# Optimization experiments

Measured on AMD Instinct MI355X. Metric: run time of the kernel, lower is better.

Reference implementation:

```python
import jax, jax.numpy as jnp
from jax import lax
import numpy as np

# ---- SLAYER SRM-alpha neuron / simulation constants (net_params) ----
THETA = 10.0      # spiking threshold
TAU_SR = 1.0      # PSP (synaptic response) time constant
TAU_REF = 1.0     # refractory time constant
TS = 1.0          # simulation timestep
POOL_GAIN = 1.1 * THETA  # SLAYER pool layer uses fixed weights = 1.1*theta (sum pool)

# SRM alpha kernel eps[n] = (n*Ts/tau) * exp(1 - n*Ts/tau) = c * n * d^n with
#   d = exp(-Ts/tau), c = e*Ts/tau.  Causal convolution with this kernel obeys
# a 2nd-order linear recurrence, so we implement psp as a lax.scan over time
# (the "recursive exponential temporal filter" the original does via temporal conv).

def psp(x):
    """Alpha-kernel temporal filter along last (time) axis."""
    d = float(np.exp(-TS / TAU_SR))
    c = float(np.e * TS / TAU_SR)
    xt = jnp.moveaxis(x, -1, 0)  # (T, ...)
    z = jnp.zeros_like(xt[0])
    def step(carry, u):
        p, q = carry
        q = d * (q + p)       # q[t] = sum_{n>=1} n d^n x[t-n]
        p = d * p + u         # p[t] = sum_{n>=0} d^n x[t-n]
        return (p, q), c * q
    _, y = lax.scan(step, (z, z), xt)
    return jnp.moveaxis(y, 0, -1)


def spike(u):
    """SLAYER spike generation: threshold the membrane potential at theta and
    subtract a refractory alpha kernel (-2*theta * alpha(tauRef)) from the
    future potential after each spike. Sequential scan over time."""
    d = float(np.exp(-TS / TAU_REF))
    c_r = float(-2.0 * THETA * np.e * TS / TAU_REF)
    ut = jnp.moveaxis(u, -1, 0)  # (T, ...)
    z = jnp.zeros_like(ut[0])
    def step(carry, u_t):
        p, q = carry
        q = d * (q + p)                       # refractory filter state
        s = (u_t + c_r * q >= THETA).astype(u_t.dtype)
        p = d * p + s                         # spikes feed the refractory filter
        return (p, q), s
    _, s = lax.scan(step, (z, z), ut)
    return jnp.moveaxis(s, 0, -1) / TS


def pool(x, k):
    """SLAYER pool: conv with fixed weight 1.1*theta (sum pool scaled)."""
    B, C, H, W, T = x.shape
    xr = x.reshape(B, C, H // k, k, W // k, k, T)
    return POOL_GAIN * xr.sum(axis=(3, 5))


def conv2d_t(x, W, pad):
    """Per-timestep 2D conv (SLAYER conv has time-kernel 1, no bias)."""
    B, C, H, Wd, T = x.shape
    xf = jnp.moveaxis(x, -1, 1).reshape(B * T, C, H, Wd)
    y = lax.conv_general_dilated(xf, W, (1, 1), [(pad, pad), (pad, pad)],
                                 dimension_numbers=('NCHW', 'OIHW', 'NCHW'))
    O, Ho, Wo = y.shape[1], y.shape[2], y.shape[3]
    return jnp.moveaxis(y.reshape(B, T, O, Ho, Wo), 1, -1)


def setup_inputs() -> dict:
    key = jax.random.key(0)
    ks = jax.random.split(key, 5)
    B, T = 8, 300
    s_in = jax.random.bernoulli(ks[0], 0.1, (B, 2, 128, 128, T)).astype(jnp.float32)
    # weightScale 10/50/... only affects init magnitude; choose scales that
    # produce non-degenerate spiking activity.
    W1 = jax.random.normal(ks[1], (16, 2, 5, 5), jnp.float32) * 0.5
    W2 = jax.random.normal(ks[2], (32, 16, 3, 3), jnp.float32) * 0.2
    Wf1 = jax.random.normal(ks[3], (512, 32, 8, 8), jnp.float32) * 0.05
    Wf2 = jax.random.normal(ks[4], (11, 512), jnp.float32) * 0.2
    return {"s_in": s_in, "W1": W1, "W2": W2, "Wf1": Wf1, "Wf2": Wf2}


def reference(s_in, W1, W2, Wf1, Wf2):
    s = spike(psp(pool(s_in, 4)))                 # SP0: (B,2,32,32,T)
    s = spike(psp(conv2d_t(s, W1, 2)))            # SC1: (B,16,32,32,T)
    s = spike(psp(pool(s, 2)))                    # SP1: (B,16,16,16,T)
    # SDC dropout p=0.0 -> identity
    s = spike(psp(conv2d_t(s, W2, 1)))            # SC2: (B,32,16,16,T)
    s = spike(psp(pool(s, 2)))                    # SP2: (B,32,8,8,T)
    # SDF dropout p=0.0 -> identity
    s = spike(psp(jnp.einsum('bchwt,ochw->bot', s, Wf1)))  # SF1: (B,512,T)
    s = spike(psp(jnp.einsum('bct,oc->bot', s, Wf2)))      # SF2: (B,11,T)
    return s
```

## Files before the change

### kernel.cpp

```cpp
#include <hip/hip_runtime.h>
#include <stdint.h>

#define T_STEPS 300
#define T4 75

typedef __attribute__((ext_vector_type(8))) short bf16x8;
typedef __attribute__((ext_vector_type(4))) float f32x4;

__device__ __forceinline__ void scan_step(float x, float& pp, float& pq,
                                          float& rp, float& rq, float& s_out) {
    const float D  = 0.36787944117144233f;
    const float C  = 2.7182818284590452f;
    const float CR = -54.365636569180904f;
    const float TH = 10.0f;
    pq = D * (pq + pp);
    pp = D * pp + x;
    float u = C * pq;
    rq = D * (rq + rp);
    float s = (u + CR * rq >= TH) ? 1.0f : 0.0f;
    rp = D * rp + s;
    s_out = s;
}

#define SCAN4(v, PACK)                                                     \
    {                                                                      \
        float s0, s1, s2, s3;                                              \
        scan_step(v.x, pp, pq, rp, rq, s0);                                \
        scan_step(v.y, pp, pq, rp, rq, s1);                                \
        scan_step(v.z, pp, pq, rp, rq, s2);                                \
        scan_step(v.w, pp, pq, rp, rq, s3);                                \
        PACK = (uint32_t)s0 | ((uint32_t)s1 << 8) |                        \
               ((uint32_t)s2 << 16) | ((uint32_t)s3 << 24);                \
    }

#define FMA4(A, wc) A.x = fmaf(wc, f0, A.x); A.y = fmaf(wc, f1, A.y); \
                    A.z = fmaf(wc, f2, A.z); A.w = fmaf(wc, f3, A.w);

__global__ __launch_bounds__(256) void k_pool4(const float* __restrict__ in,
                                               float* __restrict__ z) {
    int idx = blockIdx.x * 256 + threadIdx.x;
    int t4 = idx % T4;
    int n  = idx / T4;
    int x = n & 31, y = (n >> 5) & 31, bc = n >> 10;
    const float* base = in + ((size_t)bc * 16384 + (size_t)(4 * y) * 128 + 4 * x) * T_STEPS + 4 * t4;
    float4 acc = {0.f, 0.f, 0.f, 0.f};
#pragma unroll
    for (int i = 0; i < 4; ++i)
#pragma unroll
        for (int j = 0; j < 4; ++j) {
            float4 v = *reinterpret_cast<const float4*>(base + ((size_t)i * 128 + j) * T_STEPS);
            acc.x += v.x; acc.y += v.y; acc.z += v.z; acc.w += v.w;
        }
    float4 o = {11.f * acc.x, 11.f * acc.y, 11.f * acc.z, 11.f * acc.w};
    *reinterpret_cast<float4*>(z + (size_t)n * T_STEPS + 4 * t4) = o;
}

__global__ __launch_bounds__(256) void k_scan_l0(const float* __restrict__ z,
                                                 uint32_t* __restrict__ sp, int N) {
    int n = blockIdx.x * 256 + threadIdx.x;
    if (n >= N) return;
    const float4* zp = reinterpret_cast<const float4*>(z + (size_t)n * T_STEPS);
    float pp = 0.f, pq = 0.f, rp = 0.f, rq = 0.f;
#pragma unroll 2
    for (int t4 = 0; t4 < T4; ++t4) {
        float4 v = zp[t4];
        uint32_t pack;
        SCAN4(v, pack);
        sp[(size_t)t4 * N + n] = pack;
    }
}

__global__ __launch_bounds__(256) void k_scan_plane(const float4* __restrict__ z,
                                                    uint32_t* __restrict__ sp, int N) {
    int n = blockIdx.x * 256 + threadIdx.x;
    if (n >= N) return;
    float pp = 0.f, pq = 0.f, rp = 0.f, rq = 0.f;
#pragma unroll 2
    for (int t4 = 0; t4 < T4; ++t4) {
        float4 v = z[(size_t)t4 * N + n];
        uint32_t pack;
        SCAN4(v, pack);
        sp[(size_t)t4 * N + n] = pack;
    }
}

__global__ __launch_bounds__(256) void k_scan_f32(const float* __restrict__ z,
                                                  float* __restrict__ s, int N, int ostride) {
    int n = blockIdx.x * blockDim.x + threadIdx.x;
    if (n >= N) return;
    const float4* zp = reinterpret_cast<const float4*>(z + (size_t)n * T_STEPS);
    float* spo = s + (size_t)n * ostride;
    float pp = 0.f, pq = 0.f, rp = 0.f, rq = 0.f;
    for (int it = 0; it < T4; ++it) {
        float4 v = zp[it];
        float4 o;
        scan_step(v.x, pp, pq, rp, rq, o.x);
        scan_step(v.y, pp, pq, rp, rq, o.y);
        scan_step(v.z, pp, pq, rp, rq, o.z);
        scan_step(v.w, pp, pq, rp, rq, o.w);
        *reinterpret_cast<float4*>(spo + it * 4) = o;
    }
}

template<int HW, int NIN, int NOUT>
__global__ __launch_bounds__(256) void k_pool2s(const uint32_t* __restrict__ sin,
                                                uint32_t* __restrict__ sout) {
    int n = blockIdx.x * 256 + threadIdx.x;
    if (n >= NOUT) return;
    int x = n % HW, y = (n / HW) % HW, bc = n / (HW * HW);
    const int W2d = HW * 2;
    const uint32_t* base0 = sin + (size_t)bc * W2d * W2d + (size_t)(2 * y) * W2d + 2 * x;
    float pp = 0.f, pq = 0.f, rp = 0.f, rq = 0.f;
#pragma unroll 2
    for (int t4 = 0; t4 < T4; ++t4) {
        const uint32_t* p = base0 + (size_t)t4 * NIN;
        uint32_t sum = p[0] + p[1] + p[W2d] + p[W2d + 1];
        float4 v;
        v.x = 11.f * (float)(sum & 0xffu);
        v.y = 11.f * (float)((sum >> 8) & 0xffu);
        v.z = 11.f * (float)((sum >> 16) & 0xffu);
        v.w = 11.f * (float)(sum >> 24);
        uint32_t pack;
        SCAN4(v, pack);
        sout[(size_t)t4 * NOUT + n] = pack;
    }
}

__global__ __launch_bounds__(256) void k_pool2s_bf(const uint32_t* __restrict__ sin,
                                                   ushort* __restrict__ sb) {
    int n = blockIdx.x * 256 + threadIdx.x;
    if (n >= 16384) return;
    int x = n & 7, y = (n >> 3) & 7, bc = n >> 6;
    const uint32_t* base0 = sin + (size_t)bc * 256 + (size_t)(2 * y) * 16 + 2 * x;
    int b = n >> 11, k = n & 2047;
    ushort* out = sb + (size_t)b * 320 * 2048 + k;
    float pp = 0.f, pq = 0.f, rp = 0.f, rq = 0.f;
    for (int t4 = 0; t4 < T4; ++t4) {
        const uint32_t* p = base0 + (size_t)t4 * 65536;
        uint32_t sum = p[0] + p[1] + p[16] + p[17];
        float4 v;
        v.x = 11.f * (float)(sum & 0xffu);
        v.y = 11.f * (float)((sum >> 8) & 0xffu);
        v.z = 11.f * (float)((sum >> 16) & 0xffu);
        v.w = 11.f * (float)(sum >> 24);
        float s0, s1, s2, s3;
        scan_step(v.x, pp, pq, rp, rq, s0);
        scan_step(v.y, pp, pq, rp, rq, s1);
        scan_step(v.z, pp, pq, rp, rq, s2);
        scan_step(v.w, pp, pq, rp, rq, s3);
        out[(size_t)(t4 * 4 + 0) * 2048] = s0 != 0.f ? 0x3F80 : 0;
        out[(size_t)(t4 * 4 + 1) * 2048] = s1 != 0.f ? 0x3F80 : 0;
        out[(size_t)(t4 * 4 + 2) * 2048] = s2 != 0.f ? 0x3F80 : 0;
        out[(size_t)(t4 * 4 + 3) * 2048] = s3 != 0.f ? 0x3F80 : 0;
    }
}

__global__ __launch_bounds__(256) void k_conv1(const uint32_t* __restrict__ s0p,
                                               const float* __restrict__ W1,
                                               float4* __restrict__ z1p) {
    __shared__ float w_lds[2][25][16];
    int bid = blockIdx.x;
    int pixblk = bid & 3;
    int t4 = (bid >> 2) % 75;
    int b  = bid / 300;
    int tid = threadIdx.x;
    for (int j = tid; j < 800; j += 256) {
        int o = j & 15, kk = (j >> 4) % 25, c = j / 400;
        w_lds[c][kk][o] = W1[(o * 2 + c) * 25 + kk];
    }
    __syncthreads();
    int pix = pixblk * 256 + tid;
    int px = pix & 31, py = pix >> 5;
    float4 acc[16];
#pragma unroll
    for (int o = 0; o < 16; ++o) acc[o] = make_float4(0.f, 0.f, 0.f, 0.f);
    const uint32_t* pb = s0p + (size_t)t4 * 16384 + (size_t)(b * 2) * 1024;
    for (int c = 0; c < 2; ++c) {
#pragma unroll
        for (int ky = 0; ky < 5; ++ky) {
            int yy = py + ky - 2;
            bool rok = (unsigned)yy < 32u;
#pragma unroll
            for (int kx = 0; kx < 5; ++kx) {
                int xx = px + kx - 2;
                uint32_t v = 0;
                if (rok && (unsigned)xx < 32u) v = pb[c * 1024 + yy * 32 + xx];
                float f0 = (float)(v & 0xffu), f1 = (float)((v >> 8) & 0xffu);
                float f2 = (float)((v >> 16) & 0xffu), f3 = (float)(v >> 24);
                int kk = ky * 5 + kx;
#pragma unroll
                for (int oo = 0; oo < 4; ++oo) {
                    float4 w4 = *reinterpret_cast<const float4*>(&w_lds[c][kk][oo * 4]);
                    FMA4(acc[oo * 4 + 0], w4.x);
                    FMA4(acc[oo * 4 + 1], w4.y);
                    FMA4(acc[oo * 4 + 2], w4.z);
                    FMA4(acc[oo * 4 + 3], w4.w);
                }
            }
        }
    }
    size_t zb = (size_t)t4 * 131072 + (size_t)(b * 16) * 1024 + pix;
#pragma unroll
    for (int o = 0; o < 16; ++o) z1p[zb + o * 1024] = acc[o];
}

__global__ __launch_bounds__(256) void k_conv2(const uint32_t* __restrict__ s2p,
                                               const float* __restrict__ W2,
                                               float4* __restrict__ z2p) {
    __shared__ float w_lds[16][9][16];
    int bid = blockIdx.x;
    int oh = bid & 1;
    int t4 = (bid >> 1) % 75;
    int b  = bid / 150;
    int tid = threadIdx.x;
    for (int j = tid; j < 2304; j += 256) {
        int o = j & 15;
        int t9 = (j >> 4) % 9;
        int c  = j / 144;
        w_lds[c][t9][o] = W2[(size_t)((oh * 16 + o) * 16 + c) * 9 + t9];
    }
    __syncthreads();
    int px = tid & 15, py = tid >> 4;
    float4 acc[16];
#pragma unroll
    for (int o = 0; o < 16; ++o) acc[o] = make_float4(0.f, 0.f, 0.f, 0.f);
    const uint32_t* pb = s2p + (size_t)t4 * 32768 + (size_t)(b * 16) * 256;
    for (int c = 0; c < 16; ++c) {
#pragma unroll
        for (int ky = 0; ky < 3; ++ky) {
            int yy = py + ky - 1;
            bool rok = (unsigned)yy < 16u;
#pragma unroll
            for (int kx = 0; kx < 3; ++kx) {
                int xx = px + kx - 1;
                uint32_t v = 0;
                if (rok && (unsigned)xx < 16u) v = pb[c * 256 + yy * 16 + xx];
                float f0 = (float)(v & 0xffu), f1 = (float)((v >> 8) & 0xffu);
                float f2 = (float)((v >> 16) & 0xffu), f3 = (float)(v >> 24);
                int t9 = ky * 3 + kx;
#pragma unroll
                for (int oo = 0; oo < 4; ++oo) {
                    float4 w4 = *reinterpret_cast<const float4*>(&w_lds[c][t9][oo * 4]);
                    FMA4(acc[oo * 4 + 0], w4.x);
                    FMA4(acc[oo * 4 + 1], w4.y);
                    FMA4(acc[oo * 4 + 2], w4.z);
                    FMA4(acc[oo * 4 + 3], w4.w);
                }
            }
        }
    }
    size_t zb = (size_t)t4 * 65536 + (size_t)(b * 32 + oh * 16) * 256 + tid;
#pragma unroll
    for (int o = 0; o < 16; ++o) z2p[zb + o * 256] = acc[o];
}

__device__ __forceinline__ ushort f2bf(float f) {
    uint32_t u = __float_as_uint(f);
    u = u + 0x7fffu + ((u >> 16) & 1u);
    return (ushort)(u >> 16);
}
__device__ __forceinline__ float bf2f(ushort h) {
    return __uint_as_float((uint32_t)h << 16);
}
__global__ __launch_bounds__(256) void k_wsplit(const float* __restrict__ W,
                                                ushort* __restrict__ Wh,
                                                ushort* __restrict__ Wm,
                                                ushort* __restrict__ Wl, int n) {
    int i = blockIdx.x * 256 + threadIdx.x;
    if (i >= n) return;
    float w = W[i];
    ushort h = f2bf(w);
    float r1 = w - bf2f(h);
    ushort m = f2bf(r1);
    float r2 = r1 - bf2f(m);
    ushort l = f2bf(r2);
    Wh[i] = h; Wm[i] = m; Wl[i] = l;
}

__device__ __forceinline__ bf16x8 ldb(const ushort* p) {
    return *reinterpret_cast<const bf16x8*>(p);
}
__global__ __launch_bounds__(256) void k_fc1_mfma(const ushort* __restrict__ Wh,
                                                  const ushort* __restrict__ Wm,
                                                  const ushort* __restrict__ Wl,
                                                  const ushort* __restrict__ sb,
                                                  float* __restrict__ z) {
    int tid = threadIdx.x, lane = tid & 63, wv = tid >> 6;
    int l15 = lane & 15, l4 = lane >> 4;
    int oA = blockIdx.x * 64 + (wv & 1) * 32 + l15;
    int t  = blockIdx.y * 32 + (wv >> 1) * 16 + l15;
    int b  = blockIdx.z;
    size_t a0 = (size_t)oA * 2048 + l4 * 8;
    size_t a1 = a0 + 16 * 2048;
    size_t bo = ((size_t)b * 320 + t) * 2048 + l4 * 8;

    f32x4 acc0 = {0.f, 0.f, 0.f, 0.f};
    f32x4 acc1 = {0.f, 0.f, 0.f, 0.f};

    bf16x8 h0 = ldb(Wh + a0), h1 = ldb(Wh + a1);
    bf16x8 m0 = ldb(Wm + a0), m1 = ldb(Wm + a1);
    bf16x8 l0 = ldb(Wl + a0), l1 = ldb(Wl + a1);
    bf16x8 bb = ldb(sb + bo);

    for (int ks = 0; ks < 64; ++ks) {
        int kn = (ks < 63) ? (ks + 1) * 32 : 0;
        bf16x8 nh0 = ldb(Wh + a0 + kn), nh1 = ldb(Wh + a1 + kn);
        bf16x8 nm0 = ldb(Wm + a0 + kn), nm1 = ldb(Wm + a1 + kn);
        bf16x8 nl0 = ldb(Wl + a0 + kn), nl1 = ldb(Wl + a1 + kn);
        bf16x8 nbb = ldb(sb + bo + kn);
        acc0 = __builtin_amdgcn_mfma_f32_16x16x32_bf16(h0, bb, acc0, 0, 0, 0);
        acc1 = __builtin_amdgcn_mfma_f32_16x16x32_bf16(h1, bb, acc1, 0, 0, 0);
        acc0 = __builtin_amdgcn_mfma_f32_16x16x32_bf16(m0, bb, acc0, 0, 0, 0);
        acc1 = __builtin_amdgcn_mfma_f32_16x16x32_bf16(m1, bb, acc1, 0, 0, 0);
        acc0 = __builtin_amdgcn_mfma_f32_16x16x32_bf16(l0, bb, acc0, 0, 0, 0);
        acc1 = __builtin_amdgcn_mfma_f32_16x16x32_bf16(l1, bb, acc1, 0, 0, 0);
        h0 = nh0; h1 = nh1; m0 = nm0; m1 = nm1; l0 = nl0; l1 = nl1; bb = nbb;
    }

    if (t < T_STEPS) {
        int orow = blockIdx.x * 64 + (wv & 1) * 32 + l4 * 4;
        float* zr = z + ((size_t)b * 512 + orow) * T_STEPS + t;
        zr[0 * T_STEPS] = acc0.x;  zr[1 * T_STEPS] = acc0.y;
        zr[2 * T_STEPS] = acc0.z;  zr[3 * T_STEPS] = acc0.w;
        float* zr2 = zr + 16 * T_STEPS;
        zr2[0 * T_STEPS] = acc1.x; zr2[1 * T_STEPS] = acc1.y;
        zr2[2 * T_STEPS] = acc1.z; zr2[3 * T_STEPS] = acc1.w;
    }
}

__global__ __launch_bounds__(256) void k_fc2(const float* __restrict__ s5,
                                             const float* __restrict__ Wf2,
                                             float* __restrict__ z) {
    int idx = blockIdx.x * 256 + threadIdx.x;
    if (idx >= 6600) return;
    int t4 = idx % T4;
    int r  = idx / T4;
    int b = r & 7, o = r >> 3;
    const float* sp = s5 + (size_t)b * 512 * T_STEPS + 4 * t4;
    const float* wp = Wf2 + (size_t)o * 512;
    float a0 = 0.f, a1 = 0.f, a2 = 0.f, a3 = 0.f;
#pragma unroll 2
    for (int k = 0; k < 512; k += 4) {
        float4 wv = *reinterpret_cast<const float4*>(wp + k);
        float4 v0 = *reinterpret_cast<const float4*>(sp + (size_t)(k + 0) * T_STEPS);
        float4 v1 = *reinterpret_cast<const float4*>(sp + (size_t)(k + 1) * T_STEPS);
        float4 v2 = *reinterpret_cast<const float4*>(sp + (size_t)(k + 2) * T_STEPS);
        float4 v3 = *reinterpret_cast<const float4*>(sp + (size_t)(k + 3) * T_STEPS);
        a0 = fmaf(wv.x, v0.x, a0); a1 = fmaf(wv.x, v0.y, a1); a2 = fmaf(wv.x, v0.z, a2); a3 = fmaf(wv.x, v0.w, a3);
        a0 = fmaf(wv.y, v1.x, a0); a1 = fmaf(wv.y, v1.y, a1); a2 = fmaf(wv.y, v1.z, a2); a3 = fmaf(wv.y, v1.w, a3);
        a0 = fmaf(wv.z, v2.x, a0); a1 = fmaf(wv.z, v2.y, a1); a2 = fmaf(wv.z, v2.z, a2); a3 = fmaf(wv.z, v2.w, a3);
        a0 = fmaf(wv.w, v3.x, a0); a1 = fmaf(wv.w, v3.y, a1); a2 = fmaf(wv.w, v3.z, a2); a3 = fmaf(wv.w, v3.w, a3);
    }
    *reinterpret_cast<float4*>(z + (size_t)(b * 11 + o) * T_STEPS + 4 * t4) = make_float4(a0, a1, a2, a3);
}

__global__ void k_zero(float* out, int n) {
    int i = blockIdx.x * 256 + threadIdx.x;
    if (i < n) out[i] = 0.f;
}

extern "C" void kernel_launch(void* const* d_in, const int* in_sizes, int n_in,
                              void* d_out, int out_size, void* d_ws, size_t ws_size,
                              hipStream_t stream) {
    const float* s_in = (const float*)d_in[0];
    const float* W1   = (const float*)d_in[1];
    const float* W2   = (const float*)d_in[2];
    const float* Wf1  = (const float*)d_in[3];
    const float* Wf2  = (const float*)d_in[4];
    float* out = (float*)d_out;

    const size_t OFF_Z  = 0;
    const size_t OFF_S0 = 157286400;
    const size_t OFF_S1 = 162201600;
    const size_t OFF_S2 = 201523200;
    const size_t OFF_S3 = 211353600;
    const size_t OFF_SB = 231014400;
    const size_t OFF_S5 = 241500160;
    const size_t OFF_WH = 246415360;
    const size_t OFF_WM = 248512512;
    const size_t OFF_WL = 250609664;
    const size_t NEEDED = 252706816;

    if (ws_size < NEEDED) {
        k_zero<<<(26400 + 255) / 256, 256, 0, stream>>>(out, 26400);
        return;
    }

    char* ws = (char*)d_ws;
    float*    Z   = (float*)(ws + OFF_Z);
    uint32_t* s0p = (uint32_t*)(ws + OFF_S0);
    uint32_t* s1p = (uint32_t*)(ws + OFF_S1);
    uint32_t* s2p = (uint32_t*)(ws + OFF_S2);
    uint32_t* s3p = (uint32_t*)(ws + OFF_S3);
    ushort*   sbf = (ushort*)(ws + OFF_SB);
    float*    s5  = (float*)(ws + OFF_S5);
    ushort*   Wh  = (ushort*)(ws + OFF_WH);
    ushort*   Wm  = (ushort*)(ws + OFF_WM);
    ushort*   Wl  = (ushort*)(ws + OFF_WL);

    k_wsplit<<<4096, 256, 0, stream>>>(Wf1, Wh, Wm, Wl, 512 * 2048);

    k_pool4<<<4800, 256, 0, stream>>>(s_in, Z);
    k_scan_l0<<<64, 256, 0, stream>>>(Z, s0p, 16384);

    k_conv1<<<2400, 256, 0, stream>>>(s0p, W1, (float4*)Z);
    k_scan_plane<<<512, 256, 0, stream>>>((const float4*)Z, s1p, 131072);

    k_pool2s<16, 131072, 32768><<<128, 256, 0, stream>>>(s1p, s2p);

    k_conv2<<<1200, 256, 0, stream>>>(s2p, W2, (float4*)Z);
    k_scan_plane<<<256, 256, 0, stream>>>((const float4*)Z, s3p, 65536);

    k_pool2s_bf<<<64, 256, 0, stream>>>(s3p, sbf);

    k_fc1_mfma<<<dim3(8, 10, 8), 256, 0, stream>>>(Wh, Wm, Wl, sbf, Z);
    k_scan_f32<<<16, 256, 0, stream>>>(Z, s5, 4096, 300);

    k_fc2<<<26, 256, 0, stream>>>(s5, Wf2, Z);
    k_scan_f32<<<1, 128, 0, stream>>>(Z, out, 88, 300);
}
```

Baseline: 989.6 us.

## Store FC1 weights and spikes in MFMA fragment order for coalesced loads

The FC1 weight split kernel and the last pool/spike kernel now write their bf16 outputs directly in the per-lane MFMA fragment layout. Each wave then reads a contiguous 1KB chunk per k-step instead of strided rows. The FC1 kernel is retiled so each wave computes 16 outputs by 32 timesteps, sharing the three weight fragments across two spike tiles rather than sharing one spike tile across two weight rows. The aim is better coalescing and less load traffic per MFMA. In exchange, the pool kernel's scattered 2-byte stores become more strided, and the workspace is assumed to have room for 20 padded time tiles.

Measured after the change: 889.0 us. -10.2%, faster.

```diff
diff --git a/kernel.cpp b/kernel.cpp
--- a/kernel.cpp
+++ b/kernel.cpp
@@ -127,13 +127,14 @@
 }
 
 __global__ __launch_bounds__(256) void k_pool2s_bf(const uint32_t* __restrict__ sin,
-                                                   ushort* __restrict__ sb) {
+                                                   ushort* __restrict__ sf) {
     int n = blockIdx.x * 256 + threadIdx.x;
     if (n >= 16384) return;
     int x = n & 7, y = (n >> 3) & 7, bc = n >> 6;
     const uint32_t* base0 = sin + (size_t)bc * 256 + (size_t)(2 * y) * 16 + 2 * x;
     int b = n >> 11, k = n & 2047;
-    ushort* out = sb + (size_t)b * 320 * 2048 + k;
+    size_t kpart = ((size_t)(k >> 5)) * 512 + (size_t)((k >> 3) & 3) * 128 + (k & 7);
+    ushort* outb = sf + (size_t)b * 20 * 64 * 512 + kpart;
     float pp = 0.f, pq = 0.f, rp = 0.f, rq = 0.f;
     for (int t4 = 0; t4 < T4; ++t4) {
         const uint32_t* p = base0 + (size_t)t4 * 65536;
@@ -148,10 +149,13 @@
         scan_step(v.y, pp, pq, rp, rq, s1);
         scan_step(v.z, pp, pq, rp, rq, s2);
         scan_step(v.w, pp, pq, rp, rq, s3);
-        out[(size_t)(t4 * 4 + 0) * 2048] = s0 != 0.f ? 0x3F80 : 0;
-        out[(size_t)(t4 * 4 + 1) * 2048] = s1 != 0.f ? 0x3F80 : 0;
-        out[(size_t)(t4 * 4 + 2) * 2048] = s2 != 0.f ? 0x3F80 : 0;
-        out[(size_t)(t4 * 4 + 3) * 2048] = s3 != 0.f ? 0x3F80 : 0;
+        float sv[4] = {s0, s1, s2, s3};
+#pragma unroll
+        for (int r = 0; r < 4; ++r) {
+            int t = t4 * 4 + r;
+            outb[((size_t)(t >> 4) * 64) * 512 + (size_t)(t & 15) * 8] =
+                sv[r] != 0.f ? (ushort)0x3F80 : (ushort)0;
+        }
     }
 }
 
@@ -262,69 +266,80 @@
 __device__ __forceinline__ float bf2f(ushort h) {
     return __uint_as_float((uint32_t)h << 16);
 }
-__global__ __launch_bounds__(256) void k_wsplit(const float* __restrict__ W,
-                                                ushort* __restrict__ Wh,
-                                                ushort* __restrict__ Wm,
-                                                ushort* __restrict__ Wl, int n) {
+__global__ __launch_bounds__(256) void k_wfrag(const float* __restrict__ W,
+                                               ushort* __restrict__ Wf) {
     int i = blockIdx.x * 256 + threadIdx.x;
-    if (i >= n) return;
+    int o = i >> 11, k = i & 2047;
     float w = W[i];
     ushort h = f2bf(w);
     float r1 = w - bf2f(h);
     ushort m = f2bf(r1);
     float r2 = r1 - bf2f(m);
     ushort l = f2bf(r2);
-    Wh[i] = h; Wm[i] = m; Wl[i] = l;
+    int lane = (((k >> 3) & 3) << 4) | (o & 15);
+    size_t base = (((size_t)(o >> 4)) * 64 + (k >> 5)) * 512 + lane * 8 + (k & 7);
+    const size_t PL = (size_t)32 * 64 * 512;
+    Wf[base] = h;
+    Wf[PL + base] = m;
+    Wf[2 * PL + base] = l;
 }
 
 __device__ __forceinline__ bf16x8 ldb(const ushort* p) {
     return *reinterpret_cast<const bf16x8*>(p);
 }
-__global__ __launch_bounds__(256) void k_fc1_mfma(const ushort* __restrict__ Wh,
-                                                  const ushort* __restrict__ Wm,
-                                                  const ushort* __restrict__ Wl,
-                                                  const ushort* __restrict__ sb,
+__global__ __launch_bounds__(256) void k_fc1_frag(const ushort* __restrict__ Wf,
+                                                  const ushort* __restrict__ sf,
                                                   float* __restrict__ z) {
-    int tid = threadIdx.x, lane = tid & 63, wv = tid >> 6;
+    int wv = threadIdx.x >> 6, lane = threadIdx.x & 63;
+    int gw = blockIdx.x * 4 + wv;
+    int R  = gw & 31;
+    int combo = gw >> 5;
+    int tp = combo % 10, b = combo / 10;
     int l15 = lane & 15, l4 = lane >> 4;
-    int oA = blockIdx.x * 64 + (wv & 1) * 32 + l15;
-    int t  = blockIdx.y * 32 + (wv >> 1) * 16 + l15;
-    int b  = blockIdx.z;
-    size_t a0 = (size_t)oA * 2048 + l4 * 8;
-    size_t a1 = a0 + 16 * 2048;
-    size_t bo = ((size_t)b * 320 + t) * 2048 + l4 * 8;
+
+    const size_t PL = (size_t)32 * 64 * 512;
+    const ushort* A0p = Wf + ((size_t)R * 64) * 512 + lane * 8;
+    const ushort* A1p = A0p + PL;
+    const ushort* A2p = A0p + 2 * PL;
+    const ushort* B0p = sf + ((size_t)(b * 20 + 2 * tp + 0) * 64) * 512 + lane * 8;
+    const ushort* B1p = B0p + (size_t)64 * 512;
 
     f32x4 acc0 = {0.f, 0.f, 0.f, 0.f};
     f32x4 acc1 = {0.f, 0.f, 0.f, 0.f};
 
-    bf16x8 h0 = ldb(Wh + a0), h1 = ldb(Wh + a1);
-    bf16x8 m0 = ldb(Wm + a0), m1 = ldb(Wm + a1);
-    bf16x8 l0 = ldb(Wl + a0), l1 = ldb(Wl + a1);
-    bf16x8 bb = ldb(sb + bo);
+    bf16x8 a0 = ldb(A0p), a1 = ldb(A1p), a2 = ldb(A2p);
+    bf16x8 b0 = ldb(B0p), b1 = ldb(B1p);
 
     for (int ks = 0; ks < 64; ++ks) {
-        int kn = (ks < 63) ? (ks + 1) * 32 : 0;
-        bf16x8 nh0 = ldb(Wh + a0 + kn), nh1 = ldb(Wh + a1 + kn);
-        bf16x8 nm0 = ldb(Wm + a0 + kn), nm1 = ldb(Wm + a1 + kn);
-        bf16x8 nl0 = ldb(Wl + a0 + kn), nl1 = ldb(Wl + a1 + kn);
-        bf16x8 nbb = ldb(sb + bo + kn);
-        acc0 = __builtin_amdgcn_mfma_f32_16x16x32_bf16(h0, bb, acc0, 0, 0, 0);
-        acc1 = __builtin_amdgcn_mfma_f32_16x16x32_bf16(h1, bb, acc1, 0, 0, 0);
-        acc0 = __builtin_amdgcn_mfma_f32_16x16x32_bf16(m0, bb, acc0, 0, 0, 0);
-        acc1 = __builtin_amdgcn_mfma_f32_16x16x32_bf16(m1, bb, acc1, 0, 0, 0);
-        acc0 = __builtin_amdgcn_mfma_f32_16x16x32_bf16(l0, bb, acc0, 0, 0, 0);
-        acc1 = __builtin_amdgcn_mfma_f32_16x16x32_bf16(l1, bb, acc1, 0, 0, 0);
-        h0 = nh0; h1 = nh1; m0 = nm0; m1 = nm1; l0 = nl0; l1 = nl1; bb = nbb;
-    }
-
-    if (t < T_STEPS) {
-        int orow = blockIdx.x * 64 + (wv & 1) * 32 + l4 * 4;
-        float* zr = z + ((size_t)b * 512 + orow) * T_STEPS + t;
-        zr[0 * T_STEPS] = acc0.x;  zr[1 * T_STEPS] = acc0.y;
-        zr[2 * T_STEPS] = acc0.z;  zr[3 * T_STEPS] = acc0.w;
-        float* zr2 = zr + 16 * T_STEPS;
-        zr2[0 * T_STEPS] = acc1.x; zr2[1 * T_STEPS] = acc1.y;
-        zr2[2 * T_STEPS] = acc1.z; zr2[3 * T_STEPS] = acc1.w;
+        int kn = (ks < 63) ? (ks + 1) * 512 : 0;
+        bf16x8 na0 = ldb(A0p + kn), na1 = ldb(A1p + kn), na2 = ldb(A2p + kn);
+        bf16x8 nb0 = ldb(B0p + kn), nb1 = ldb(B1p + kn);
+        acc0 = __builtin_amdgcn_mfma_f32_16x16x32_bf16(a0, b0, acc0, 0, 0, 0);
+        acc1 = __builtin_amdgcn_mfma_f32_16x16x32_bf16(a0, b1, acc1, 0, 0, 0);
+        acc0 = __builtin_amdgcn_mfma_f32_16x16x32_bf16(a1, b0, acc0, 0, 0, 0);
+        acc1 = __builtin_amdgcn_mfma_f32_16x16x32_bf16(a1, b1, acc1, 0, 0, 0);
+        acc0 = __builtin_amdgcn_mfma_f32_16x16x32_bf16(a2, b0, acc0, 0, 0, 0);
+        acc1 = __builtin_amdgcn_mfma_f32_16x16x32_bf16(a2, b1, acc1, 0, 0, 0);
+        a0 = na0; a1 = na1; a2 = na2; b0 = nb0; b1 = nb1;
+    }
+
+    int orow = R * 16 + l4 * 4;
+    int tb = tp * 32;
+    {
+        int tc = tb + l15;
+        if (tc < T_STEPS) {
+            float* zr = z + ((size_t)b * 512 + orow) * T_STEPS + tc;
+            zr[0 * T_STEPS] = acc0.x; zr[1 * T_STEPS] = acc0.y;
+            zr[2 * T_STEPS] = acc0.z; zr[3 * T_STEPS] = acc0.w;
+        }
+    }
+    {
+        int tc = tb + 16 + l15;
+        if (tc < T_STEPS) {
+            float* zr = z + ((size_t)b * 512 + orow) * T_STEPS + tc;
+            zr[0 * T_STEPS] = acc1.x; zr[1 * T_STEPS] = acc1.y;
+            zr[2 * T_STEPS] = acc1.z; zr[3 * T_STEPS] = acc1.w;
+        }
     }
 }
 
@@ -376,9 +391,7 @@
     const size_t OFF_S3 = 211353600;
     const size_t OFF_SB = 231014400;
     const size_t OFF_S5 = 241500160;
-    const size_t OFF_WH = 246415360;
-    const size_t OFF_WM = 248512512;
-    const size_t OFF_WL = 250609664;
+    const size_t OFF_WF = 246415360;
     const size_t NEEDED = 252706816;
 
     if (ws_size < NEEDED) {
@@ -394,11 +407,9 @@
     uint32_t* s3p = (uint32_t*)(ws + OFF_S3);
     ushort*   sbf = (ushort*)(ws + OFF_SB);
     float*    s5  = (float*)(ws + OFF_S5);
-    ushort*   Wh  = (ushort*)(ws + OFF_WH);
-    ushort*   Wm  = (ushort*)(ws + OFF_WM);
-    ushort*   Wl  = (ushort*)(ws + OFF_WL);
-
-    k_wsplit<<<4096, 256, 0, stream>>>(Wf1, Wh, Wm, Wl, 512 * 2048);
+    ushort*   Wfr = (ushort*)(ws + OFF_WF);
+
+    k_wfrag<<<4096, 256, 0, stream>>>(Wf1, Wfr);
 
     k_pool4<<<4800, 256, 0, stream>>>(s_in, Z);
     k_scan_l0<<<64, 256, 0, stream>>>(Z, s0p, 16384);
@@ -413,7 +424,7 @@
 
     k_pool2s_bf<<<64, 256, 0, stream>>>(s3p, sbf);
 
-    k_fc1_mfma<<<dim3(8, 10, 8), 256, 0, stream>>>(Wh, Wm, Wl, sbf, Z);
+    k_fc1_frag<<<640, 256, 0, stream>>>(Wfr, sbf, Z);
     k_scan_f32<<<16, 256, 0, stream>>>(Z, s5, 4096, 300);
 
     k_fc2<<<26, 256, 0, stream>>>(s5, Wf2, Z);
```
